# Optimization experiments

Measured on AMD Instinct MI355X. Metric: run time of the kernel, lower is better.

The kernel has to match this reference:

```python
import jax, jax.numpy as jnp
import numpy as np

B, T, H, NSPK = 8, 1024, 1024, 2
LN_EPS = 1e-5


def setup_inputs() -> dict:
    key = jax.random.key(0)
    ks = jax.random.split(key, 12)
    s = 1.0 / np.sqrt(H)
    return {
        "x": jax.random.normal(ks[0], (B, T, H), jnp.float32),
        "qmask": jax.random.uniform(ks[1], (B, T, NSPK), jnp.float32),
        "dia_len": jax.random.randint(ks[2], (B,), T // 2, T + 1),
        "wp": 8,
        "wf": 8,
        "W_msg": jax.random.normal(ks[3], (H, H), jnp.float32) * s,
        "b_msg": jax.random.normal(ks[4], (H,), jnp.float32) * s,
        "W_self": jax.random.normal(ks[5], (H, H), jnp.float32) * s,
        "b_self": jax.random.normal(ks[6], (H,), jnp.float32) * s,
        "W_out": jax.random.normal(ks[7], (H, H), jnp.float32) * s,
        "b_out": jax.random.normal(ks[8], (H,), jnp.float32) * s,
        "gamma": jnp.ones((H,), jnp.float32),
        "beta": jnp.zeros((H,), jnp.float32),
    }


def reference(x, qmask, dia_len, wp, wf, W_msg, b_msg, W_self, b_self, W_out, b_out, gamma, beta):
    Bb, Tt, Hh = x.shape
    spk = jnp.argmax(qmask, axis=-1)                     # [B,T]
    pos = jnp.arange(Tt)
    offs = jnp.arange(-wp, wf + 1)                       # [W]
    idx = pos[:, None] + offs[None, :]                   # [T,W] window indices
    vlen = dia_len[:, None, None]                        # [B,1,1]
    valid = (idx[None] >= 0) & (idx[None] <= vlen - 1)   # [B,T,W]
    idxc = jnp.clip(idx, 0, Tt - 1)
    nb = jnp.take(x, idxc, axis=1)                       # [B,T,W,H]
    nb_spk = jnp.take(spk, idxc, axis=1)                 # [B,T,W]
    same = (nb_spk == spk[:, :, None]).astype(x.dtype)
    w = jnp.where(valid, 0.5 + 0.5 * same, 0.0)          # speaker weights, masked
    cnt = jnp.maximum(valid.sum(-1).astype(x.dtype), 1.0)  # window sizes [B,T]
    msg = jnp.einsum('btw,btwh->bth', w, nb) / cnt[..., None]
    h = x @ W_self + b_self + msg @ W_msg + b_msg        # per-node fusion
    node_valid = (pos[None, :] < dia_len[:, None])[..., None]
    out = jnp.where(node_valid, h, x)                    # nodes past dia_len keep x
    y = jax.nn.relu(out) @ W_out + b_out                 # dropout = identity (eval)
    z = x + y
    mean = z.mean(-1, keepdims=True)
    var = z.var(-1, keepdims=True)
    return gamma * (z - mean) / jnp.sqrt(var + LN_EPS) + beta
```

## Files before the change

kernel.cpp:

```cpp
#include <hip/hip_runtime.h>


typedef unsigned short u16;
typedef float floatx4 __attribute__((ext_vector_type(4)));
typedef short shortx8 __attribute__((ext_vector_type(8)));

#define T_ 1024
#define H_ 1024

__device__ __forceinline__ float bf2f(u16 v) {
    return __uint_as_float(((unsigned)v) << 16);
}
__device__ __forceinline__ u16 f2bf(float f) {
    unsigned u = __float_as_uint(f);
    return (u16)((u + 0x7fffu + ((u >> 16) & 1u)) >> 16);
}
__device__ __forceinline__ void async16(const void* g, void* l) {
    __builtin_amdgcn_global_load_lds(
        (__attribute__((address_space(1))) void*)g,
        (__attribute__((address_space(3))) void*)l, 16, 0, 0);
}
__device__ __forceinline__ void barrier_mem() {
    asm volatile("" ::: "memory");
    __builtin_amdgcn_s_barrier();
    asm volatile("" ::: "memory");
}

__global__ __launch_bounds__(256)
void prep_kernel(const float* __restrict__ x, const float* __restrict__ qmask,
                 const int* __restrict__ dia_len,
                 const float* __restrict__ Wself, const float* __restrict__ Wmsg,
                 const float* __restrict__ Wout,
                 u16* __restrict__ xcat, u16* __restrict__ wt_cat,
                 u16* __restrict__ wt_out)
{
    __shared__ u16 sx[32][1024];
    const int tid = threadIdx.x;
    const int bx = blockIdx.x;

    if (bx >= 512) {
        const int id = bx - 512;
        const int wid = id >> 10;
        const int rest = id & 1023;
        const int n0 = (rest & 31) * 32, k0 = (rest >> 5) * 32;
        const float* src = (wid == 0) ? Wself : ((wid == 1) ? Wmsg : Wout);
        float (*s)[33] = reinterpret_cast<float (*)[33]>(&sx[0][0]);
        const int tx = tid & 31, ty = tid >> 5;
#pragma unroll
        for (int i = 0; i < 4; ++i) {
            int k = k0 + ty + 8 * i;
            s[ty + 8 * i][tx] = src[(size_t)k * H_ + n0 + tx];
        }
        __syncthreads();
#pragma unroll
        for (int i = 0; i < 4; ++i) {
            int n = n0 + ty + 8 * i;
            u16 v = f2bf(s[tx][ty + 8 * i]);
            if (wid < 2) wt_cat[(size_t)n * 2048 + wid * 1024 + k0 + tx] = v;
            else         wt_out[(size_t)n * 1024 + k0 + tx] = v;
        }
        return;
    }

    const int b = bx >> 6;
    const int t0 = (bx & 63) * 16;
    const int dlen = dia_len[b];
    const int c4 = tid * 4;
    const float* xb = x + (size_t)b * T_ * H_;

    unsigned spkmask = 0;
#pragma unroll 4
    for (int r = 0; r < 32; ++r) {
        int row = t0 - 8 + r;
        row = row < 0 ? 0 : (row > T_ - 1 ? T_ - 1 : row);
        const float* q = qmask + ((size_t)b * T_ + row) * 2;
        spkmask |= (q[1] > q[0] ? 1u : 0u) << r;
        float4 v = *(const float4*)(xb + (size_t)row * H_ + c4);
        ushort4 u;
        u.x = f2bf(v.x); u.y = f2bf(v.y); u.z = f2bf(v.z); u.w = f2bf(v.w);
        *(ushort4*)&sx[r][c4] = u;
    }
    __syncthreads();

    for (int lt = 0; lt < 16; ++lt) {
        const int t = t0 + lt;
        const unsigned cs = (spkmask >> (lt + 8)) & 1u;
        float a0 = 0.f, a1 = 0.f, a2 = 0.f, a3 = 0.f;
        int cnt = 0;
#pragma unroll
        for (int o = 0; o < 17; ++o) {
            const int idx = t + o - 8;
            if (idx >= 0 && idx < dlen) {
                const float w = (((spkmask >> (lt + o)) & 1u) == cs) ? 1.0f : 0.5f;
                ++cnt;
                ushort4 u = *(const ushort4*)&sx[lt + o][c4];
                a0 += w * bf2f(u.x); a1 += w * bf2f(u.y);
                a2 += w * bf2f(u.z); a3 += w * bf2f(u.w);
            }
        }
        const float inv = 1.0f / (float)(cnt > 0 ? cnt : 1);
        ushort4 m;
        m.x = f2bf(a0 * inv); m.y = f2bf(a1 * inv);
        m.z = f2bf(a2 * inv); m.w = f2bf(a3 * inv);
        const size_t rowg = (size_t)b * T_ + t;
        *(ushort4*)&xcat[rowg * 2048 + 1024 + c4] = m;
        *(ushort4*)&xcat[rowg * 2048 + c4] = *(const ushort4*)&sx[lt + 8][c4];
    }
}

template <int K, int EPI>
__global__ __launch_bounds__(512, 4)
void gemm_bt(const u16* __restrict__ A, const u16* __restrict__ Bt,
             const float* __restrict__ bias1, const float* __restrict__ bias2,
             const float* __restrict__ X, const int* __restrict__ dia_len,
             u16* __restrict__ Rout, float* __restrict__ Zout)
{
    constexpr int NT = K / 64;
    static_assert(NT >= 2, "need >=2 K-tiles");
    __shared__ u16 sA[2][128 * 64];
    __shared__ u16 sB[2][128 * 64];
    const int tid = threadIdx.x;

    const int bid = blockIdx.x;
    const int xcd = bid & 7, li = bid >> 3;
    const int mt = xcd * 8 + (li >> 3);
    const int nt = li & 7;
    const int bm = mt * 128, bn = nt * 128;

    const int wave = tid >> 6, lane = tid & 63;
    const int wr = wave >> 1, wc = wave & 1;
    const int lrow = lane & 15, lq = lane >> 4;

    const int srow = tid >> 3;
    const int sl   = (tid & 7) ^ (srow & 7);
    const u16* Asrc = A + (size_t)(bm + srow) * K + sl * 8;
    const u16* Bsrc = Bt + (size_t)(bn + srow) * K + sl * 8;

    auto stage = [&](int t, int buf) {
        const int k0 = t * 64;
        async16(Asrc + k0,                    &sA[buf][tid * 8]);
        async16(Asrc + (size_t)64 * K + k0,   &sA[buf][4096 + tid * 8]);
        async16(Bsrc + k0,                    &sB[buf][tid * 8]);
        async16(Bsrc + (size_t)64 * K + k0,   &sB[buf][4096 + tid * 8]);
    };

    floatx4 acc[2][4];
#pragma unroll
    for (int i = 0; i < 2; ++i)
#pragma unroll
        for (int j = 0; j < 4; ++j)
            acc[i][j] = (floatx4){0.f, 0.f, 0.f, 0.f};

    const int xk = lrow & 7;
    const int paBase = (wr * 32 + lrow) * 64;
    const int pbBase = (wc * 64 + lrow) * 64;
    const int s0 = (lq ^ xk) * 8;
    const int s1 = ((4 + lq) ^ xk) * 8;

    stage(0, 0);
    stage(1, 1);
    asm volatile("s_waitcnt vmcnt(4)" ::: "memory");
    barrier_mem();

    for (int t = 0; t < NT; ++t) {
        if (t >= 1 && t + 1 < NT) stage(t + 1, (t + 1) & 1);

        const u16* curA = &sA[t & 1][0];
        const u16* curB = &sB[t & 1][0];
        shortx8 a0[2], a1[2], b0[4], b1[4];
#pragma unroll
        for (int j = 0; j < 4; ++j)
            b0[j] = *(const shortx8*)(curB + pbBase + j * 1024 + s0);
#pragma unroll
        for (int i = 0; i < 2; ++i)
            a0[i] = *(const shortx8*)(curA + paBase + i * 1024 + s0);
#pragma unroll
        for (int j = 0; j < 4; ++j)
            b1[j] = *(const shortx8*)(curB + pbBase + j * 1024 + s1);
#pragma unroll
        for (int i = 0; i < 2; ++i)
            a1[i] = *(const shortx8*)(curA + paBase + i * 1024 + s1);

        __builtin_amdgcn_s_setprio(1);
#pragma unroll
        for (int i = 0; i < 2; ++i)
#pragma unroll
            for (int j = 0; j < 4; ++j)
                acc[i][j] = __builtin_amdgcn_mfma_f32_16x16x32_bf16(
                    a0[i], b0[j], acc[i][j], 0, 0, 0);
#pragma unroll
        for (int i = 0; i < 2; ++i)
#pragma unroll
            for (int j = 0; j < 4; ++j)
                acc[i][j] = __builtin_amdgcn_mfma_f32_16x16x32_bf16(
                    a1[i], b1[j], acc[i][j], 0, 0, 0);
        __builtin_amdgcn_s_setprio(0);

        if (t + 1 < NT) {
            asm volatile("s_waitcnt vmcnt(0)" ::: "memory");
            barrier_mem();
        }
    }

    const int dl = (EPI == 1) ? dia_len[bm >> 10] : 0;
#pragma unroll
    for (int i = 0; i < 2; ++i) {
        const int row0 = bm + wr * 32 + i * 16 + lq * 4;
#pragma unroll
        for (int j = 0; j < 4; ++j) {
            const int col = bn + wc * 64 + j * 16 + lrow;
#pragma unroll
            for (int r = 0; r < 4; ++r) {
                const int row = row0 + r;
                const float v = acc[i][j][r];
                if (EPI == 1) {
                    const float h = v + bias1[col] + bias2[col];
                    float outv;
                    if ((row & (T_ - 1)) < dl) {
                        outv = h;
                    } else {
                        outv = X[(size_t)row * H_ + col];
                    }
                    Rout[(size_t)row * H_ + col] = f2bf(fmaxf(outv, 0.f));
                } else {
                    const float z = X[(size_t)row * H_ + col] + v + bias1[col];
                    Zout[(size_t)row * H_ + col] = z;
                }
            }
        }
    }
}

__global__ __launch_bounds__(256)
void ln_kernel(const float* __restrict__ Z, const float* __restrict__ gamma,
               const float* __restrict__ beta, float* __restrict__ out)
{
    const int row = blockIdx.x;
    const int tid = threadIdx.x;
    const size_t base = (size_t)row * H_ + tid * 4;
    float4 v = *(const float4*)(Z + base);
    float s = v.x + v.y + v.z + v.w;
    float q = v.x * v.x + v.y * v.y + v.z * v.z + v.w * v.w;
#pragma unroll
    for (int off = 32; off > 0; off >>= 1) {
        s += __shfl_down(s, off);
        q += __shfl_down(q, off);
    }
    __shared__ float ps[4], pq[4];
    const int wave = tid >> 6, lane = tid & 63;
    if (lane == 0) { ps[wave] = s; pq[wave] = q; }
    __syncthreads();
    const float S = ps[0] + ps[1] + ps[2] + ps[3];
    const float Q = pq[0] + pq[1] + pq[2] + pq[3];
    const float mean = S * (1.0f / 1024.0f);
    const float var = Q * (1.0f / 1024.0f) - mean * mean;
    const float inv = rsqrtf(var + 1e-5f);
    float4 g = *(const float4*)(gamma + tid * 4);
    float4 bt = *(const float4*)(beta + tid * 4);
    float4 o;
    o.x = g.x * (v.x - mean) * inv + bt.x;
    o.y = g.y * (v.y - mean) * inv + bt.y;
    o.z = g.z * (v.z - mean) * inv + bt.z;
    o.w = g.w * (v.w - mean) * inv + bt.w;
    *(float4*)(out + base) = o;
}

extern "C" void kernel_launch(void* const* d_in, const int* in_sizes, int n_in,
                              void* d_out, int out_size, void* d_ws, size_t ws_size,
                              hipStream_t stream)
{
    (void)in_sizes; (void)n_in; (void)out_size; (void)ws_size;
    const float* x       = (const float*)d_in[0];
    const float* qmask   = (const float*)d_in[1];
    const int*   dia_len = (const int*)d_in[2];
    const float* W_msg   = (const float*)d_in[5];
    const float* b_msg   = (const float*)d_in[6];
    const float* W_self  = (const float*)d_in[7];
    const float* b_self  = (const float*)d_in[8];
    const float* W_out   = (const float*)d_in[9];
    const float* b_out   = (const float*)d_in[10];
    const float* gamma   = (const float*)d_in[11];
    const float* beta    = (const float*)d_in[12];
    float* out = (float*)d_out;

    char* ws = (char*)d_ws;
    u16*   xcat   = (u16*)ws;
    u16*   rbuf   = (u16*)(ws + (size_t)(32u << 20));
    u16*   wt_cat = (u16*)(ws + (size_t)(48u << 20));
    u16*   wt_out = (u16*)(ws + (size_t)(52u << 20));
    float* zbuf   = (float*)ws;

    prep_kernel<<<dim3(3584), 256, 0, stream>>>(x, qmask, dia_len,
                                                W_self, W_msg, W_out,
                                                xcat, wt_cat, wt_out);
    gemm_bt<2048, 1><<<dim3(512), 512, 0, stream>>>(xcat, wt_cat, b_self, b_msg,
                                                    x, dia_len, rbuf, nullptr);
    gemm_bt<1024, 2><<<dim3(512), 512, 0, stream>>>(rbuf, wt_out, b_out, nullptr,
                                                    x, nullptr, nullptr, zbuf);
    ln_kernel<<<dim3(8192), 256, 0, stream>>>(zbuf, gamma, beta, out);
}
```

Baseline: 206.4 us.

## Deepen GEMM pipeline to 4-stage K=32 tiles with register double-buffering

Splits the GEMM K loop into 32-wide tiles held in a 4-slot LDS ring, issuing async global-to-LDS loads three tiles ahead and waiting with a partial vmcnt instead of draining all loads. LDS fragments for the next tile are read into a second register set while the current tile's MFMAs run, with a sched_barrier to keep that order. The aim is to hide global and LDS latency behind compute. In exchange there are twice as many barriers per K, a new XOR swizzle whose bank-conflict behaviour is unproven, and more register pressure.

```diff
diff --git a/kernel.cpp b/kernel.cpp
--- a/kernel.cpp
+++ b/kernel.cpp
@@ -108,6 +108,39 @@
     }
 }
 
+
+#define LOADSET(AV, BV, TT) do {                                              \
+    const u16* pA_ = &sA[(TT) & 3][0];                                        \
+    const u16* pB_ = &sB[(TT) & 3][0];                                        \
+    AV[0] = *(const shortx8*)(pA_ + aOff0);                                   \
+    AV[1] = *(const shortx8*)(pA_ + aOff1);                                   \
+    BV[0] = *(const shortx8*)(pB_ + bOff0);                                   \
+    BV[1] = *(const shortx8*)(pB_ + bOff1);                                   \
+    BV[2] = *(const shortx8*)(pB_ + bOff2);                                   \
+    BV[3] = *(const shortx8*)(pB_ + bOff3);                                   \
+} while (0)
+
+#define GBODY(TT, AC, BC, AN, BNV) do {                                       \
+    if ((TT) + 1 < NT) LOADSET(AN, BNV, (TT) + 1);                            \
+    if ((TT) + 3 < NT) stage((TT) + 3);                                       \
+    __builtin_amdgcn_sched_barrier(0);                                        \
+    __builtin_amdgcn_s_setprio(1);                                            \
+    acc[0][0] = __builtin_amdgcn_mfma_f32_16x16x32_bf16(AC[0], BC[0], acc[0][0], 0, 0, 0); \
+    acc[1][0] = __builtin_amdgcn_mfma_f32_16x16x32_bf16(AC[1], BC[0], acc[1][0], 0, 0, 0); \
+    acc[0][1] = __builtin_amdgcn_mfma_f32_16x16x32_bf16(AC[0], BC[1], acc[0][1], 0, 0, 0); \
+    acc[1][1] = __builtin_amdgcn_mfma_f32_16x16x32_bf16(AC[1], BC[1], acc[1][1], 0, 0, 0); \
+    acc[0][2] = __builtin_amdgcn_mfma_f32_16x16x32_bf16(AC[0], BC[2], acc[0][2], 0, 0, 0); \
+    acc[1][2] = __builtin_amdgcn_mfma_f32_16x16x32_bf16(AC[1], BC[2], acc[1][2], 0, 0, 0); \
+    acc[0][3] = __builtin_amdgcn_mfma_f32_16x16x32_bf16(AC[0], BC[3], acc[0][3], 0, 0, 0); \
+    acc[1][3] = __builtin_amdgcn_mfma_f32_16x16x32_bf16(AC[1], BC[3], acc[1][3], 0, 0, 0); \
+    __builtin_amdgcn_s_setprio(0);                                            \
+    if ((TT) + 1 < NT) {                                                      \
+        if ((TT) + 3 < NT) asm volatile("s_waitcnt vmcnt(2)" ::: "memory");   \
+        else               asm volatile("s_waitcnt vmcnt(0)" ::: "memory");   \
+        barrier_mem();                                                        \
+    }                                                                         \
+} while (0)
+
 template <int K, int EPI>
 __global__ __launch_bounds__(512, 4)
 void gemm_bt(const u16* __restrict__ A, const u16* __restrict__ Bt,
@@ -115,10 +148,10 @@
              const float* __restrict__ X, const int* __restrict__ dia_len,
              u16* __restrict__ Rout, float* __restrict__ Zout)
 {
-    constexpr int NT = K / 64;
-    static_assert(NT >= 2, "need >=2 K-tiles");
-    __shared__ u16 sA[2][128 * 64];
-    __shared__ u16 sB[2][128 * 64];
+    constexpr int NT = K / 32;
+    static_assert(NT >= 4 && (NT & 1) == 0, "NT even, >=4");
+    __shared__ u16 sA[4][128 * 32];
+    __shared__ u16 sB[4][128 * 32];
     const int tid = threadIdx.x;
 
     const int bid = blockIdx.x;
@@ -131,17 +164,15 @@
     const int wr = wave >> 1, wc = wave & 1;
     const int lrow = lane & 15, lq = lane >> 4;
 
-    const int srow = tid >> 3;
-    const int sl   = (tid & 7) ^ (srow & 7);
+    const int srow = tid >> 2;
+    const int sl   = (tid & 3) ^ ((srow >> 1) & 3);
     const u16* Asrc = A + (size_t)(bm + srow) * K + sl * 8;
     const u16* Bsrc = Bt + (size_t)(bn + srow) * K + sl * 8;
 
-    auto stage = [&](int t, int buf) {
-        const int k0 = t * 64;
-        async16(Asrc + k0,                    &sA[buf][tid * 8]);
-        async16(Asrc + (size_t)64 * K + k0,   &sA[buf][4096 + tid * 8]);
-        async16(Bsrc + k0,                    &sB[buf][tid * 8]);
-        async16(Bsrc + (size_t)64 * K + k0,   &sB[buf][4096 + tid * 8]);
+    auto stage = [&](int t) {
+        const int s = t & 3;
+        async16(Asrc + t * 32, &sA[s][tid * 8]);
+        async16(Bsrc + t * 32, &sB[s][tid * 8]);
     };
 
     floatx4 acc[2][4];
@@ -151,55 +182,26 @@
         for (int j = 0; j < 4; ++j)
             acc[i][j] = (floatx4){0.f, 0.f, 0.f, 0.f};
 
-    const int xk = lrow & 7;
-    const int paBase = (wr * 32 + lrow) * 64;
-    const int pbBase = (wc * 64 + lrow) * 64;
-    const int s0 = (lq ^ xk) * 8;
-    const int s1 = ((4 + lq) ^ xk) * 8;
-
-    stage(0, 0);
-    stage(1, 1);
-    asm volatile("s_waitcnt vmcnt(4)" ::: "memory");
+    const int ra0 = wr * 32 + lrow,      ra1 = ra0 + 16;
+    const int rb0 = wc * 64 + lrow,      rb1 = rb0 + 16,
+              rb2 = rb0 + 32,            rb3 = rb0 + 48;
+    const int aOff0 = ra0 * 32 + (lq ^ ((ra0 >> 1) & 3)) * 8;
+    const int aOff1 = ra1 * 32 + (lq ^ ((ra1 >> 1) & 3)) * 8;
+    const int bOff0 = rb0 * 32 + (lq ^ ((rb0 >> 1) & 3)) * 8;
+    const int bOff1 = rb1 * 32 + (lq ^ ((rb1 >> 1) & 3)) * 8;
+    const int bOff2 = rb2 * 32 + (lq ^ ((rb2 >> 1) & 3)) * 8;
+    const int bOff3 = rb3 * 32 + (lq ^ ((rb3 >> 1) & 3)) * 8;
+
+    stage(0); stage(1); stage(2);
+    asm volatile("s_waitcnt vmcnt(2)" ::: "memory");
     barrier_mem();
 
-    for (int t = 0; t < NT; ++t) {
-        if (t >= 1 && t + 1 < NT) stage(t + 1, (t + 1) & 1);
-
-        const u16* curA = &sA[t & 1][0];
-        const u16* curB = &sB[t & 1][0];
-        shortx8 a0[2], a1[2], b0[4], b1[4];
-#pragma unroll
-        for (int j = 0; j < 4; ++j)
-            b0[j] = *(const shortx8*)(curB + pbBase + j * 1024 + s0);
-#pragma unroll
-        for (int i = 0; i < 2; ++i)
-            a0[i] = *(const shortx8*)(curA + paBase + i * 1024 + s0);
-#pragma unroll
-        for (int j = 0; j < 4; ++j)
-            b1[j] = *(const shortx8*)(curB + pbBase + j * 1024 + s1);
-#pragma unroll
-        for (int i = 0; i < 2; ++i)
-            a1[i] = *(const shortx8*)(curA + paBase + i * 1024 + s1);
-
-        __builtin_amdgcn_s_setprio(1);
-#pragma unroll
-        for (int i = 0; i < 2; ++i)
-#pragma unroll
-            for (int j = 0; j < 4; ++j)
-                acc[i][j] = __builtin_amdgcn_mfma_f32_16x16x32_bf16(
-                    a0[i], b0[j], acc[i][j], 0, 0, 0);
-#pragma unroll
-        for (int i = 0; i < 2; ++i)
-#pragma unroll
-            for (int j = 0; j < 4; ++j)
-                acc[i][j] = __builtin_amdgcn_mfma_f32_16x16x32_bf16(
-                    a1[i], b1[j], acc[i][j], 0, 0, 0);
-        __builtin_amdgcn_s_setprio(0);
-
-        if (t + 1 < NT) {
-            asm volatile("s_waitcnt vmcnt(0)" ::: "memory");
-            barrier_mem();
-        }
+    shortx8 aP[2], bP[4], aQ[2], bQ[4];
+    LOADSET(aP, bP, 0);
+
+    for (int t = 0; t < NT; t += 2) {
+        GBODY(t,     aP, bP, aQ, bQ);
+        GBODY(t + 1, aQ, bQ, aP, bP);
     }
 
     const int dl = (EPI == 1) ? dia_len[bm >> 10] : 0;
```

New measurement: 210.7 us. 1.02x slower.

## Split GEMM K-tile across wave groups and stage epilogue through LDS

Applied to the files above, without the earlier changes.

The 8 waves are regrouped into two K-groups that each compute a full 64x64 quadrant over half of each 64-wide K tile, with 4x4 accumulators per wave instead of 2x4. This cuts per-wave LDS fragment loads relative to the MFMA work. The partial sums are reduced through shared memory, and the epilogue then writes coalesced vector stores to Rout/Zout instead of strided scalar stores. The cost is doubled accumulator registers, which may hurt occupancy under launch_bounds(512,4), plus extra barriers and LDS traffic in the epilogue.

```diff
diff --git a/kernel.cpp b/kernel.cpp
--- a/kernel.cpp
+++ b/kernel.cpp
@@ -117,8 +117,10 @@
 {
     constexpr int NT = K / 64;
     static_assert(NT >= 2, "need >=2 K-tiles");
-    __shared__ u16 sA[2][128 * 64];
-    __shared__ u16 sB[2][128 * 64];
+    __shared__ char smem[65536];
+    u16* sA = (u16*)smem;
+    u16* sB = (u16*)(smem + 32768);
+    float* ef = (float*)smem;
     const int tid = threadIdx.x;
 
     const int bid = blockIdx.x;
@@ -128,7 +130,8 @@
     const int bm = mt * 128, bn = nt * 128;
 
     const int wave = tid >> 6, lane = tid & 63;
-    const int wr = wave >> 1, wc = wave & 1;
+    const int kg = wave >> 2;
+    const int wr = (wave >> 1) & 1, wc = wave & 1;
     const int lrow = lane & 15, lq = lane >> 4;
 
     const int srow = tid >> 3;
@@ -138,24 +141,28 @@
 
     auto stage = [&](int t, int buf) {
         const int k0 = t * 64;
-        async16(Asrc + k0,                    &sA[buf][tid * 8]);
-        async16(Asrc + (size_t)64 * K + k0,   &sA[buf][4096 + tid * 8]);
-        async16(Bsrc + k0,                    &sB[buf][tid * 8]);
-        async16(Bsrc + (size_t)64 * K + k0,   &sB[buf][4096 + tid * 8]);
+        async16(Asrc + k0,                  sA + buf * 8192 + tid * 8);
+        async16(Asrc + (size_t)64 * K + k0, sA + buf * 8192 + 4096 + tid * 8);
+        async16(Bsrc + k0,                  sB + buf * 8192 + tid * 8);
+        async16(Bsrc + (size_t)64 * K + k0, sB + buf * 8192 + 4096 + tid * 8);
     };
 
-    floatx4 acc[2][4];
-#pragma unroll
-    for (int i = 0; i < 2; ++i)
+    floatx4 acc[4][4];
+#pragma unroll
+    for (int i = 0; i < 4; ++i)
 #pragma unroll
         for (int j = 0; j < 4; ++j)
             acc[i][j] = (floatx4){0.f, 0.f, 0.f, 0.f};
 
     const int xk = lrow & 7;
-    const int paBase = (wr * 32 + lrow) * 64;
-    const int pbBase = (wc * 64 + lrow) * 64;
-    const int s0 = (lq ^ xk) * 8;
-    const int s1 = ((4 + lq) ^ xk) * 8;
+    const int ks = ((kg * 4 + lq) ^ xk) * 8;
+    int aOff[4], bOff[4];
+#pragma unroll
+    for (int i = 0; i < 4; ++i)
+        aOff[i] = (wr * 64 + i * 16 + lrow) * 64 + ks;
+#pragma unroll
+    for (int j = 0; j < 4; ++j)
+        bOff[j] = (wc * 64 + j * 16 + lrow) * 64 + ks;
 
     stage(0, 0);
     stage(1, 1);
@@ -165,35 +172,21 @@
     for (int t = 0; t < NT; ++t) {
         if (t >= 1 && t + 1 < NT) stage(t + 1, (t + 1) & 1);
 
-        const u16* curA = &sA[t & 1][0];
-        const u16* curB = &sB[t & 1][0];
-        shortx8 a0[2], a1[2], b0[4], b1[4];
-#pragma unroll
-        for (int j = 0; j < 4; ++j)
-            b0[j] = *(const shortx8*)(curB + pbBase + j * 1024 + s0);
-#pragma unroll
-        for (int i = 0; i < 2; ++i)
-            a0[i] = *(const shortx8*)(curA + paBase + i * 1024 + s0);
-#pragma unroll
-        for (int j = 0; j < 4; ++j)
-            b1[j] = *(const shortx8*)(curB + pbBase + j * 1024 + s1);
-#pragma unroll
-        for (int i = 0; i < 2; ++i)
-            a1[i] = *(const shortx8*)(curA + paBase + i * 1024 + s1);
+        const u16* cA = sA + (t & 1) * 8192;
+        const u16* cB = sB + (t & 1) * 8192;
+        shortx8 av[4], bv[4];
+#pragma unroll
+        for (int j = 0; j < 4; ++j) bv[j] = *(const shortx8*)(cB + bOff[j]);
+#pragma unroll
+        for (int i = 0; i < 4; ++i) av[i] = *(const shortx8*)(cA + aOff[i]);
 
         __builtin_amdgcn_s_setprio(1);
 #pragma unroll
-        for (int i = 0; i < 2; ++i)
+        for (int i = 0; i < 4; ++i)
 #pragma unroll
             for (int j = 0; j < 4; ++j)
                 acc[i][j] = __builtin_amdgcn_mfma_f32_16x16x32_bf16(
-                    a0[i], b0[j], acc[i][j], 0, 0, 0);
-#pragma unroll
-        for (int i = 0; i < 2; ++i)
-#pragma unroll
-            for (int j = 0; j < 4; ++j)
-                acc[i][j] = __builtin_amdgcn_mfma_f32_16x16x32_bf16(
-                    a1[i], b1[j], acc[i][j], 0, 0, 0);
+                    av[i], bv[j], acc[i][j], 0, 0, 0);
         __builtin_amdgcn_s_setprio(0);
 
         if (t + 1 < NT) {
@@ -202,32 +195,87 @@
         }
     }
 
+    __syncthreads();
     const int dl = (EPI == 1) ? dia_len[bm >> 10] : 0;
-#pragma unroll
-    for (int i = 0; i < 2; ++i) {
-        const int row0 = bm + wr * 32 + i * 16 + lq * 4;
-#pragma unroll
-        for (int j = 0; j < 4; ++j) {
-            const int col = bn + wc * 64 + j * 16 + lrow;
-#pragma unroll
-            for (int r = 0; r < 4; ++r) {
-                const int row = row0 + r;
-                const float v = acc[i][j][r];
-                if (EPI == 1) {
-                    const float h = v + bias1[col] + bias2[col];
-                    float outv;
-                    if ((row & (T_ - 1)) < dl) {
-                        outv = h;
-                    } else {
-                        outv = X[(size_t)row * H_ + col];
-                    }
-                    Rout[(size_t)row * H_ + col] = f2bf(fmaxf(outv, 0.f));
-                } else {
-                    const float z = X[(size_t)row * H_ + col] + v + bias1[col];
-                    Zout[(size_t)row * H_ + col] = z;
-                }
-            }
-        }
+
+    for (int s = 0; s < 2; ++s) {
+        if (kg == 0 && wr == s) {
+#pragma unroll
+            for (int j = 0; j < 4; ++j) {
+                const int lc = wc * 64 + j * 16 + lrow;
+                const float bb = (EPI == 1) ? bias1[bn + lc] + bias2[bn + lc]
+                                            : bias1[bn + lc];
+#pragma unroll
+                for (int i = 0; i < 4; ++i)
+#pragma unroll
+                    for (int r = 0; r < 4; ++r)
+                        ef[(i * 16 + lq * 4 + r) * 132 + lc] = acc[i][j][r] + bb;
+            }
+        }
+        __syncthreads();
+        if (kg == 1 && wr == s) {
+#pragma unroll
+            for (int j = 0; j < 4; ++j) {
+                const int lc = wc * 64 + j * 16 + lrow;
+#pragma unroll
+                for (int i = 0; i < 4; ++i)
+#pragma unroll
+                    for (int r = 0; r < 4; ++r)
+                        ef[(i * 16 + lq * 4 + r) * 132 + lc] += acc[i][j][r];
+            }
+        }
+        __syncthreads();
+        if (EPI == 1) {
+            const int lr = tid >> 3, sg = tid & 7;
+            const int row = bm + s * 64 + lr;
+            const int gcol = bn + sg * 16;
+            shortx8 w0, w1;
+            if ((row & (T_ - 1)) < dl) {
+                const float* ep = ef + lr * 132 + sg * 16;
+                float4 e0 = *(const float4*)(ep);
+                float4 e1 = *(const float4*)(ep + 4);
+                float4 e2 = *(const float4*)(ep + 8);
+                float4 e3 = *(const float4*)(ep + 12);
+                w0[0] = (short)f2bf(fmaxf(e0.x, 0.f)); w0[1] = (short)f2bf(fmaxf(e0.y, 0.f));
+                w0[2] = (short)f2bf(fmaxf(e0.z, 0.f)); w0[3] = (short)f2bf(fmaxf(e0.w, 0.f));
+                w0[4] = (short)f2bf(fmaxf(e1.x, 0.f)); w0[5] = (short)f2bf(fmaxf(e1.y, 0.f));
+                w0[6] = (short)f2bf(fmaxf(e1.z, 0.f)); w0[7] = (short)f2bf(fmaxf(e1.w, 0.f));
+                w1[0] = (short)f2bf(fmaxf(e2.x, 0.f)); w1[1] = (short)f2bf(fmaxf(e2.y, 0.f));
+                w1[2] = (short)f2bf(fmaxf(e2.z, 0.f)); w1[3] = (short)f2bf(fmaxf(e2.w, 0.f));
+                w1[4] = (short)f2bf(fmaxf(e3.x, 0.f)); w1[5] = (short)f2bf(fmaxf(e3.y, 0.f));
+                w1[6] = (short)f2bf(fmaxf(e3.z, 0.f)); w1[7] = (short)f2bf(fmaxf(e3.w, 0.f));
+            } else {
+                const float* xp = X + (size_t)row * H_ + gcol;
+                float4 x0 = *(const float4*)(xp);
+                float4 x1 = *(const float4*)(xp + 4);
+                float4 x2 = *(const float4*)(xp + 8);
+                float4 x3 = *(const float4*)(xp + 12);
+                w0[0] = (short)f2bf(fmaxf(x0.x, 0.f)); w0[1] = (short)f2bf(fmaxf(x0.y, 0.f));
+                w0[2] = (short)f2bf(fmaxf(x0.z, 0.f)); w0[3] = (short)f2bf(fmaxf(x0.w, 0.f));
+                w0[4] = (short)f2bf(fmaxf(x1.x, 0.f)); w0[5] = (short)f2bf(fmaxf(x1.y, 0.f));
+                w0[6] = (short)f2bf(fmaxf(x1.z, 0.f)); w0[7] = (short)f2bf(fmaxf(x1.w, 0.f));
+                w1[0] = (short)f2bf(fmaxf(x2.x, 0.f)); w1[1] = (short)f2bf(fmaxf(x2.y, 0.f));
+                w1[2] = (short)f2bf(fmaxf(x2.z, 0.f)); w1[3] = (short)f2bf(fmaxf(x2.w, 0.f));
+                w1[4] = (short)f2bf(fmaxf(x3.x, 0.f)); w1[5] = (short)f2bf(fmaxf(x3.y, 0.f));
+                w1[6] = (short)f2bf(fmaxf(x3.z, 0.f)); w1[7] = (short)f2bf(fmaxf(x3.w, 0.f));
+            }
+            u16* rp = Rout + (size_t)row * H_ + gcol;
+            *(shortx8*)(rp) = w0;
+            *(shortx8*)(rp + 8) = w1;
+        } else {
+#pragma unroll
+            for (int k = 0; k < 4; ++k) {
+                const int idx = tid + k * 512;
+                const int lr = idx >> 5, sg = idx & 31;
+                const int row = bm + s * 64 + lr;
+                const int gcol = bn + sg * 4;
+                float4 zv = *(const float4*)&ef[lr * 132 + sg * 4];
+                float4 xv = *(const float4*)(X + (size_t)row * H_ + gcol);
+                zv.x += xv.x; zv.y += xv.y; zv.z += xv.z; zv.w += xv.w;
+                *(float4*)(Zout + (size_t)row * H_ + gcol) = zv;
+            }
+        }
+        __syncthreads();
     }
 }
 
```

New measurement: 202.6 us. No clear change (-1.9%).
